# Optimization experiments

Hardware: AMD Instinct MI355X
Metric: run time of the kernel (lower is better)

Reference implementation:

```python
import jax, jax.numpy as jnp
import numpy as np

HID = (128, 256, 128)  # nmp_qc NNet hidden layer sizes
D_IN = 256
TARGET = 256


def _mlp_params(key, n_in, n_out, prefix):
    sizes = (n_in,) + HID + (n_out,)
    params = {}
    for i in range(len(sizes) - 1):
        key, k1, k2 = jax.random.split(key, 3)
        fan_in = sizes[i]
        bound = 1.0 / np.sqrt(fan_in)
        params[f"{prefix}_W{i}"] = jax.random.uniform(k1, (sizes[i], sizes[i + 1]), jnp.float32, -bound, bound)
        params[f"{prefix}_b{i}"] = jax.random.uniform(k2, (sizes[i + 1],), jnp.float32, -bound, bound)
    return params, key


def _mlp(x, Ws, bs):
    # ReLU on all layers except the last (linear output), matching NNet
    for i in range(len(Ws) - 1):
        x = jax.nn.relu(x @ Ws[i] + bs[i])
    return x @ Ws[-1] + bs[-1]


def setup_inputs() -> dict:
    key = jax.random.key(0)
    k0, k1, key = jax.random.split(key, 3)
    B, N = 512, 256
    inp = {
        "h0": jax.random.normal(k0, (B, N, D_IN), jnp.float32),
        "hT": jax.random.normal(k1, (B, N, D_IN), jnp.float32),
    }
    gp, key = _mlp_params(key, 2 * D_IN, TARGET, "g")  # gate MLP: concat(h0,hT) -> target
    op, key = _mlp_params(key, D_IN, TARGET, "o")      # value MLP: hT -> target
    inp.update(gp)
    inp.update(op)
    return inp


def reference(h0, hT,
              g_W0, g_b0, g_W1, g_b1, g_W2, g_b2, g_W3, g_b3,
              o_W0, o_b0, o_W1, o_b1, o_W2, o_b2, o_W3, o_b3):
    gWs = (g_W0, g_W1, g_W2, g_W3)
    gbs = (g_b0, g_b1, g_b2, g_b3)
    oWs = (o_W0, o_W1, o_W2, o_W3)
    obs = (o_b0, o_b1, o_b2, o_b3)
    # gate: sigmoid(MLP1([h0; hT])) ; value: MLP2(hT)  -- all [B, N, target]
    gate = jax.nn.sigmoid(_mlp(jnp.concatenate([h0, hT], axis=-1), gWs, gbs))
    val = _mlp(hT, oWs, obs)
    # node validity mask: sum of initial features > 0, matching r_mpnn
    mask = (jnp.sum(h0, axis=-1, keepdims=True) > 0).astype(h0.dtype)  # [B, N, 1]
    return jnp.sum(mask * gate * val, axis=1)  # [B, target]
```

## Files before the change

### kernel.cpp

```cpp
#include <hip/hip_runtime.h>
#include <hip/hip_bf16.h>
#include <stdint.h>


typedef __attribute__((ext_vector_type(8))) short short8_t;
typedef __attribute__((ext_vector_type(4))) float f32x4;

#define ROWS      48
#define TOTROWS   131072
#define NWG       2731

#define OFF_R     0
#define P_ELEMS   (48*136)
#define OFF_A     26112
#define OFF_B1    39168
#define OFF_MASK  63744
#define LDS_TOTAL 63936

__device__ __forceinline__ short f2bf(float f) {
  union { float f; uint32_t u; } v; v.f = f;
  uint32_t r = (v.u + 0x7FFFu + ((v.u >> 16) & 1u)) >> 16;
  return (short)r;
}
__device__ __forceinline__ float bf2f(short b) {
  union { uint32_t u; float f; } v; v.u = ((uint32_t)(uint16_t)b) << 16;
  return v.f;
}

template <int KTOT, int KSTEPS, int CT>
__device__ __forceinline__ void gemm_block(const short* __restrict__ actin, int Sin,
                                           const short* __restrict__ wsB, int kbaseB,
                                           f32x4 (&acc)[3][CT], int wv, int m, int q) {
#pragma unroll
  for (int ks = 0; ks < KSTEPS; ++ks) {
    const int kl = ks * 32 + q * 8;
    short8_t b[CT];
#pragma unroll
    for (int ct = 0; ct < CT; ++ct) {
      const int n = wv * (CT * 16) + ct * 16 + m;
      b[ct] = *(const short8_t*)(wsB + n * KTOT + kbaseB + kl);
    }
    short8_t a[3];
#pragma unroll
    for (int rt = 0; rt < 3; ++rt)
      a[rt] = *(const short8_t*)(actin + (rt * 16 + m) * Sin + kl);
#pragma unroll
    for (int ct = 0; ct < CT; ++ct)
#pragma unroll
      for (int rt = 0; rt < 3; ++rt)
        acc[rt][ct] = __builtin_amdgcn_mfma_f32_16x16x32_bf16(a[rt], b[ct], acc[rt][ct], 0, 0, 0);
  }
}

template <int N, int ACTF>
__device__ __forceinline__ void epilogue(f32x4 (&acc)[3][N / 64], short* actout, int Sout,
                                         const float* __restrict__ bias, int wv, int m, int q) {
  constexpr int CT = N / 64;
#pragma unroll
  for (int ct = 0; ct < CT; ++ct) {
    const int c = wv * (CT * 16) + ct * 16 + m;
    const float bv = bias[c];
#pragma unroll
    for (int rt = 0; rt < 3; ++rt)
#pragma unroll
      for (int i = 0; i < 4; ++i) {
        float v = acc[rt][ct][i] + bv;
        if (ACTF == 1) v = fmaxf(v, 0.f);
        if (ACTF == 2) v = 1.f / (1.f + __expf(-v));
        actout[(rt * 16 + q * 4 + i) * Sout + c] = f2bf(v);
      }
  }
}

template <int K, int N, int ACTF>
__device__ __forceinline__ void layer(const short* actin, int Sin, short* actout, int Sout,
                                      const short* __restrict__ wsB, const float* __restrict__ bias,
                                      int wv, int m, int q) {
  constexpr int CT = N / 64;
  f32x4 acc[3][CT];
#pragma unroll
  for (int rt = 0; rt < 3; ++rt)
#pragma unroll
    for (int ct = 0; ct < CT; ++ct) acc[rt][ct] = (f32x4)(0.f);
  gemm_block<K, K / 32, CT>(actin, Sin, wsB, 0, acc, wv, m, q);
  epilogue<N, ACTF>(acc, actout, Sout, bias, wv, m, q);
}

__device__ __forceinline__ void stage_load(const float* __restrict__ src, int row0, int colbase,
                                           int tid, float4 (&v)[6]) {
  const int c4 = tid & 31, rb = tid >> 5;
#pragma unroll
  for (int it = 0; it < 6; ++it) {
    int gr = row0 + rb + it * 8;
    if (gr >= TOTROWS) gr = TOTROWS - 1;
    v[it] = *(const float4*)(src + (size_t)gr * 256 + colbase + c4 * 4);
  }
}

__device__ __forceinline__ void stage_store(short* Pb, int tid, const float4 (&v)[6],
                                            float* maskacc, int mmode) {
  const int c4 = tid & 31, rb = tid >> 5;
#pragma unroll
  for (int it = 0; it < 6; ++it) {
    const int r = rb + it * 8;
    short4 pk; pk.x = f2bf(v[it].x); pk.y = f2bf(v[it].y); pk.z = f2bf(v[it].z); pk.w = f2bf(v[it].w);
    *(short4*)(Pb + r * 136 + c4 * 4) = pk;
    if (mmode) {
      float s = v[it].x + v[it].y + v[it].z + v[it].w;
      s += __shfl_down(s, 16, 32);
      s += __shfl_down(s, 8, 32);
      s += __shfl_down(s, 4, 32);
      s += __shfl_down(s, 2, 32);
      s += __shfl_down(s, 1, 32);
      if (c4 == 0) {
        if (mmode == 1) maskacc[r] = s; else maskacc[r] += s;
      }
    }
  }
}

template <int NCH, bool MASKA>
__device__ __forceinline__ void stream_layer(const float* __restrict__ src0,
                                             const float* __restrict__ src1, int splitc,
                                             const short* __restrict__ wsB,
                                             const float* __restrict__ bias,
                                             short* P, short* Aout, float* maskacc,
                                             int row0, int tid, int wv, int m, int q) {
  constexpr int KTOT = NCH * 128;
  f32x4 acc[3][2];
#pragma unroll
  for (int rt = 0; rt < 3; ++rt)
#pragma unroll
    for (int ct = 0; ct < 2; ++ct) acc[rt][ct] = (f32x4)(0.f);

  float4 v[6];
  stage_load(src0, row0, 0, tid, v);
  stage_store(P, tid, v, maskacc, MASKA ? 1 : 0);
  __syncthreads();
#pragma unroll
  for (int kc = 0; kc < NCH; ++kc) {
    const bool more = (kc + 1 < NCH);
    if (more) {
      const bool lo = (kc + 1 < splitc);
      stage_load(lo ? src0 : src1, row0, (lo ? (kc + 1) : (kc + 1 - splitc)) * 128, tid, v);
    }
    gemm_block<KTOT, 4, 2>(P + (kc & 1) * P_ELEMS, 136, wsB, kc * 128, acc, wv, m, q);
    if (more) {
      const int mm = (MASKA && (kc + 1 < splitc)) ? 2 : 0;
      stage_store(P + ((kc + 1) & 1) * P_ELEMS, tid, v, maskacc, mm);
    }
    __syncthreads();
  }
  epilogue<128, 1>(acc, Aout, 136, bias, wv, m, q);
}

__device__ __forceinline__ void final_layer(const short* actin, const short* __restrict__ wsB,
                                            const float* __restrict__ bias,
                                            const short* gateB, const float* maskacc,
                                            float* __restrict__ out, int row0,
                                            int wv, int m, int q) {
  f32x4 acc[3][4];
#pragma unroll
  for (int rt = 0; rt < 3; ++rt)
#pragma unroll
    for (int ct = 0; ct < 4; ++ct) acc[rt][ct] = (f32x4)(0.f);
  gemm_block<128, 4, 4>(actin, 136, wsB, 0, acc, wv, m, q);

  const int b0 = row0 >> 8;
  const int b1 = (row0 + ROWS - 1) >> 8;
#pragma unroll
  for (int ct = 0; ct < 4; ++ct) {
    const int c = wv * 64 + ct * 16 + m;
    const float bv = bias[c];
    float p0 = 0.f, p1 = 0.f;
#pragma unroll
    for (int rt = 0; rt < 3; ++rt)
#pragma unroll
      for (int i = 0; i < 4; ++i) {
        const int r = rt * 16 + q * 4 + i;
        const int gr = row0 + r;
        const float vv = acc[rt][ct][i] + bv;
        const float g = bf2f(gateB[r * 256 + c]);
        float contrib = (gr < TOTROWS && maskacc[r] > 0.f) ? g * vv : 0.f;
        if ((gr >> 8) == b0) p0 += contrib; else p1 += contrib;
      }
    p0 += __shfl_down(p0, 32); p0 += __shfl_down(p0, 16);
    p1 += __shfl_down(p1, 32); p1 += __shfl_down(p1, 16);
    if (q == 0) {
      atomicAdd(out + b0 * 256 + c, p0);
      if (b1 != b0 && b1 < 512) atomicAdd(out + b1 * 256 + c, p1);
    }
  }
}

__global__ __launch_bounds__(256, 2)
void readout_main(const float* __restrict__ h0, const float* __restrict__ hT,
                  const short* __restrict__ ws,
                  const float* __restrict__ gb0, const float* __restrict__ gb1,
                  const float* __restrict__ gb2, const float* __restrict__ gb3,
                  const float* __restrict__ ob0, const float* __restrict__ ob1,
                  const float* __restrict__ ob2, const float* __restrict__ ob3,
                  float* __restrict__ out) {
  __shared__ __align__(16) char smem[LDS_TOTAL];
  short* P  = (short*)(smem + OFF_R);
  short* B2 = (short*)(smem + OFF_R);
  short* A  = (short*)(smem + OFF_A);
  short* B1 = (short*)(smem + OFF_B1);
  float* maskacc = (float*)(smem + OFF_MASK);

  const int tid = threadIdx.x;
  const int wv = tid >> 6, lane = tid & 63;
  const int m = lane & 15, q = lane >> 4;
  const int row0 = blockIdx.x * ROWS;

  stream_layer<4, true>(h0, hT, 2, ws + 0, gb0, P, A, maskacc, row0, tid, wv, m, q);
  __syncthreads();
  layer<128, 256, 1>(A, 136, B2, 264, ws + 65536, gb1, wv, m, q);
  __syncthreads();
  layer<256, 128, 1>(B2, 264, A, 136, ws + 98304, gb2, wv, m, q);
  __syncthreads();
  layer<128, 256, 2>(A, 136, B1, 256, ws + 131072, gb3, wv, m, q);
  __syncthreads();
  stream_layer<2, false>(hT, hT, 2, ws + 163840, ob0, P, A, maskacc, row0, tid, wv, m, q);
  __syncthreads();
  layer<128, 256, 1>(A, 136, B2, 264, ws + 196608, ob1, wv, m, q);
  __syncthreads();
  layer<256, 128, 1>(B2, 264, A, 136, ws + 229376, ob2, wv, m, q);
  __syncthreads();
  final_layer(A, ws + 262144, ob3, B1, maskacc, out, row0, wv, m, q);
}

__global__ void prep(const float* __restrict__ W0, const float* __restrict__ W1,
                     const float* __restrict__ W2, const float* __restrict__ W3,
                     const float* __restrict__ W4, const float* __restrict__ W5,
                     const float* __restrict__ W6, const float* __restrict__ W7,
                     short* __restrict__ ws, float* __restrict__ out) {
  const int l = blockIdx.y;
  const int le = blockIdx.x * 256 + threadIdx.x;
  if (l == 1) { out[le] = 0.f; out[le + 65536] = 0.f; }
  int K, N, off; const float* W;
  switch (l) {
    case 0:  K = 512; N = 128; off = 0;      W = W0; break;
    case 1:  K = 128; N = 256; off = 65536;  W = W1; break;
    case 2:  K = 256; N = 128; off = 98304;  W = W2; break;
    case 3:  K = 128; N = 256; off = 131072; W = W3; break;
    case 4:  K = 256; N = 128; off = 163840; W = W4; break;
    case 5:  K = 128; N = 256; off = 196608; W = W5; break;
    case 6:  K = 256; N = 128; off = 229376; W = W6; break;
    default: K = 128; N = 256; off = 262144; W = W7; break;
  }
  if (le >= K * N) return;
  const int k = le / N, n = le % N;
  ws[off + n * K + k] = f2bf(W[le]);
}

extern "C" void kernel_launch(void* const* d_in, const int* in_sizes, int n_in,
                              void* d_out, int out_size, void* d_ws, size_t ws_size,
                              hipStream_t stream) {
  const float* h0  = (const float*)d_in[0];
  const float* hT  = (const float*)d_in[1];
  const float* gW0 = (const float*)d_in[2];  const float* gb0 = (const float*)d_in[3];
  const float* gW1 = (const float*)d_in[4];  const float* gb1 = (const float*)d_in[5];
  const float* gW2 = (const float*)d_in[6];  const float* gb2 = (const float*)d_in[7];
  const float* gW3 = (const float*)d_in[8];  const float* gb3 = (const float*)d_in[9];
  const float* oW0 = (const float*)d_in[10]; const float* ob0 = (const float*)d_in[11];
  const float* oW1 = (const float*)d_in[12]; const float* ob1 = (const float*)d_in[13];
  const float* oW2 = (const float*)d_in[14]; const float* ob2 = (const float*)d_in[15];
  const float* oW3 = (const float*)d_in[16]; const float* ob3 = (const float*)d_in[17];
  float* out = (float*)d_out;
  short* ws  = (short*)d_ws;

  prep<<<dim3(256, 8), 256, 0, stream>>>(gW0, gW1, gW2, gW3, oW0, oW1, oW2, oW3, ws, out);
  readout_main<<<NWG, 256, 0, stream>>>(h0, hT, ws,
                                        gb0, gb1, gb2, gb3,
                                        ob0, ob1, ob2, ob3, out);
}
```

Baseline: 520.8 us.

## Switch to 32x32 MFMA tiles, 64-row blocks, and keep gate output in registers

Result: faster. 483.3 us (-7.2%).

```diff
diff --git a/kernel.cpp b/kernel.cpp
--- a/kernel.cpp
+++ b/kernel.cpp
@@ -4,18 +4,16 @@
 
 
 typedef __attribute__((ext_vector_type(8))) short short8_t;
-typedef __attribute__((ext_vector_type(4))) float f32x4;
-
-#define ROWS      48
-#define TOTROWS   131072
-#define NWG       2731
-
-#define OFF_R     0
-#define P_ELEMS   (48*136)
-#define OFF_A     26112
-#define OFF_B1    39168
-#define OFF_MASK  63744
-#define LDS_TOTAL 63936
+typedef __attribute__((ext_vector_type(16))) float f32x16;
+
+#define ROWS 64
+#define NWG  2048
+
+#define PE        (64 * 136)
+#define OFF_P     0
+#define OFF_A     34816
+#define OFF_MASK  52224
+#define LDS_TOTAL 52480
 
 __device__ __forceinline__ short f2bf(float f) {
   union { float f; uint32_t u; } v; v.f = f;
@@ -28,80 +26,76 @@
 }
 
 template <int KTOT, int KSTEPS, int CT>
-__device__ __forceinline__ void gemm_block(const short* __restrict__ actin, int Sin,
-                                           const short* __restrict__ wsB, int kbaseB,
-                                           f32x4 (&acc)[3][CT], int wv, int m, int q) {
+__device__ __forceinline__ void gemm32(const short* actin, int Sin,
+                                       const short* __restrict__ wsB, int kw0, int c0,
+                                       f32x16 (&acc)[2][CT], int n32, int q32) {
 #pragma unroll
   for (int ks = 0; ks < KSTEPS; ++ks) {
-    const int kl = ks * 32 + q * 8;
+    const int kl = ks * 16 + q32 * 8;
     short8_t b[CT];
 #pragma unroll
-    for (int ct = 0; ct < CT; ++ct) {
-      const int n = wv * (CT * 16) + ct * 16 + m;
-      b[ct] = *(const short8_t*)(wsB + n * KTOT + kbaseB + kl);
-    }
-    short8_t a[3];
-#pragma unroll
-    for (int rt = 0; rt < 3; ++rt)
-      a[rt] = *(const short8_t*)(actin + (rt * 16 + m) * Sin + kl);
-#pragma unroll
     for (int ct = 0; ct < CT; ++ct)
-#pragma unroll
-      for (int rt = 0; rt < 3; ++rt)
-        acc[rt][ct] = __builtin_amdgcn_mfma_f32_16x16x32_bf16(a[rt], b[ct], acc[rt][ct], 0, 0, 0);
-  }
-}
-
-template <int N, int ACTF>
-__device__ __forceinline__ void epilogue(f32x4 (&acc)[3][N / 64], short* actout, int Sout,
-                                         const float* __restrict__ bias, int wv, int m, int q) {
-  constexpr int CT = N / 64;
+      b[ct] = *(const short8_t*)(wsB + (size_t)(c0 + ct * 32 + n32) * KTOT + kw0 + kl);
+    short8_t a[2];
+#pragma unroll
+    for (int rt = 0; rt < 2; ++rt)
+      a[rt] = *(const short8_t*)(actin + (rt * 32 + n32) * Sin + kl);
+#pragma unroll
+    for (int ct = 0; ct < CT; ++ct)
+#pragma unroll
+      for (int rt = 0; rt < 2; ++rt)
+        acc[rt][ct] = __builtin_amdgcn_mfma_f32_32x32x16_bf16(a[rt], b[ct], acc[rt][ct], 0, 0, 0);
+  }
+}
+
+template <int CT, int ACTF>
+__device__ __forceinline__ void epi32(f32x16 (&acc)[2][CT], short* actout, int Sout,
+                                      const float* __restrict__ bias, int c0, int n32, int q32) {
 #pragma unroll
   for (int ct = 0; ct < CT; ++ct) {
-    const int c = wv * (CT * 16) + ct * 16 + m;
+    const int c = c0 + ct * 32 + n32;
     const float bv = bias[c];
 #pragma unroll
-    for (int rt = 0; rt < 3; ++rt)
-#pragma unroll
-      for (int i = 0; i < 4; ++i) {
-        float v = acc[rt][ct][i] + bv;
+    for (int rt = 0; rt < 2; ++rt)
+#pragma unroll
+      for (int reg = 0; reg < 16; ++reg) {
+        const int r = rt * 32 + (reg & 3) + 8 * (reg >> 2) + 4 * q32;
+        float v = acc[rt][ct][reg] + bv;
         if (ACTF == 1) v = fmaxf(v, 0.f);
-        if (ACTF == 2) v = 1.f / (1.f + __expf(-v));
-        actout[(rt * 16 + q * 4 + i) * Sout + c] = f2bf(v);
+        actout[r * Sout + c] = f2bf(v);
       }
   }
 }
 
 template <int K, int N, int ACTF>
-__device__ __forceinline__ void layer(const short* actin, int Sin, short* actout, int Sout,
-                                      const short* __restrict__ wsB, const float* __restrict__ bias,
-                                      int wv, int m, int q) {
-  constexpr int CT = N / 64;
-  f32x4 acc[3][CT];
-#pragma unroll
-  for (int rt = 0; rt < 3; ++rt)
-#pragma unroll
-    for (int ct = 0; ct < CT; ++ct) acc[rt][ct] = (f32x4)(0.f);
-  gemm_block<K, K / 32, CT>(actin, Sin, wsB, 0, acc, wv, m, q);
-  epilogue<N, ACTF>(acc, actout, Sout, bias, wv, m, q);
+__device__ __forceinline__ void layer32(const short* actin, int Sin, short* actout, int Sout,
+                                        const short* __restrict__ wsB,
+                                        const float* __restrict__ bias,
+                                        int wv, int n32, int q32) {
+  constexpr int CT = N / 128;
+  const int c0 = wv * (N / 4);
+  f32x16 acc[2][CT];
+#pragma unroll
+  for (int rt = 0; rt < 2; ++rt)
+#pragma unroll
+    for (int ct = 0; ct < CT; ++ct) acc[rt][ct] = (f32x16)(0.f);
+  gemm32<K, K / 16, CT>(actin, Sin, wsB, 0, c0, acc, n32, q32);
+  epi32<CT, ACTF>(acc, actout, Sout, bias, c0, n32, q32);
 }
 
 __device__ __forceinline__ void stage_load(const float* __restrict__ src, int row0, int colbase,
-                                           int tid, float4 (&v)[6]) {
+                                           int tid, float4 (&v)[8]) {
   const int c4 = tid & 31, rb = tid >> 5;
 #pragma unroll
-  for (int it = 0; it < 6; ++it) {
-    int gr = row0 + rb + it * 8;
-    if (gr >= TOTROWS) gr = TOTROWS - 1;
-    v[it] = *(const float4*)(src + (size_t)gr * 256 + colbase + c4 * 4);
-  }
-}
-
-__device__ __forceinline__ void stage_store(short* Pb, int tid, const float4 (&v)[6],
+  for (int it = 0; it < 8; ++it)
+    v[it] = *(const float4*)(src + (size_t)(row0 + rb + it * 8) * 256 + colbase + c4 * 4);
+}
+
+__device__ __forceinline__ void stage_store(short* Pb, int tid, const float4 (&v)[8],
                                             float* maskacc, int mmode) {
   const int c4 = tid & 31, rb = tid >> 5;
 #pragma unroll
-  for (int it = 0; it < 6; ++it) {
+  for (int it = 0; it < 8; ++it) {
     const int r = rb + it * 8;
     short4 pk; pk.x = f2bf(v[it].x); pk.y = f2bf(v[it].y); pk.z = f2bf(v[it].z); pk.w = f2bf(v[it].w);
     *(short4*)(Pb + r * 136 + c4 * 4) = pk;
@@ -120,80 +114,93 @@
 }
 
 template <int NCH, bool MASKA>
-__device__ __forceinline__ void stream_layer(const float* __restrict__ src0,
-                                             const float* __restrict__ src1, int splitc,
-                                             const short* __restrict__ wsB,
-                                             const float* __restrict__ bias,
-                                             short* P, short* Aout, float* maskacc,
-                                             int row0, int tid, int wv, int m, int q) {
+__device__ __forceinline__ void stream32(const float* __restrict__ src0,
+                                         const float* __restrict__ src1, int splitc,
+                                         const short* __restrict__ wsB,
+                                         const float* __restrict__ bias,
+                                         short* P, short* Aout, float* maskacc,
+                                         int row0, int tid, int wv, int n32, int q32) {
   constexpr int KTOT = NCH * 128;
-  f32x4 acc[3][2];
-#pragma unroll
-  for (int rt = 0; rt < 3; ++rt)
-#pragma unroll
-    for (int ct = 0; ct < 2; ++ct) acc[rt][ct] = (f32x4)(0.f);
-
-  float4 v[6];
+  f32x16 acc[2][1];
+  acc[0][0] = (f32x16)(0.f); acc[1][0] = (f32x16)(0.f);
+  float4 v[8];
   stage_load(src0, row0, 0, tid, v);
   stage_store(P, tid, v, maskacc, MASKA ? 1 : 0);
   __syncthreads();
 #pragma unroll
   for (int kc = 0; kc < NCH; ++kc) {
-    const bool more = (kc + 1 < NCH);
-    if (more) {
+    if (kc + 1 < NCH) {
       const bool lo = (kc + 1 < splitc);
-      stage_load(lo ? src0 : src1, row0, (lo ? (kc + 1) : (kc + 1 - splitc)) * 128, tid, v);
+      stage_load(lo ? src0 : src1, row0, (lo ? kc + 1 : kc + 1 - splitc) * 128, tid, v);
     }
-    gemm_block<KTOT, 4, 2>(P + (kc & 1) * P_ELEMS, 136, wsB, kc * 128, acc, wv, m, q);
-    if (more) {
-      const int mm = (MASKA && (kc + 1 < splitc)) ? 2 : 0;
-      stage_store(P + ((kc + 1) & 1) * P_ELEMS, tid, v, maskacc, mm);
-    }
+    gemm32<KTOT, 8, 1>(P + (kc & 1) * PE, 136, wsB, kc * 128, wv * 32, acc, n32, q32);
+    if (kc + 1 < NCH)
+      stage_store(P + ((kc + 1) & 1) * PE, tid, v, maskacc, (MASKA && kc + 1 < splitc) ? 2 : 0);
     __syncthreads();
   }
-  epilogue<128, 1>(acc, Aout, 136, bias, wv, m, q);
-}
-
-__device__ __forceinline__ void final_layer(const short* actin, const short* __restrict__ wsB,
-                                            const float* __restrict__ bias,
-                                            const short* gateB, const float* maskacc,
-                                            float* __restrict__ out, int row0,
-                                            int wv, int m, int q) {
-  f32x4 acc[3][4];
-#pragma unroll
-  for (int rt = 0; rt < 3; ++rt)
-#pragma unroll
-    for (int ct = 0; ct < 4; ++ct) acc[rt][ct] = (f32x4)(0.f);
-  gemm_block<128, 4, 4>(actin, 136, wsB, 0, acc, wv, m, q);
-
-  const int b0 = row0 >> 8;
-  const int b1 = (row0 + ROWS - 1) >> 8;
-#pragma unroll
-  for (int ct = 0; ct < 4; ++ct) {
-    const int c = wv * 64 + ct * 16 + m;
+  epi32<1, 1>(acc, Aout, 136, bias, wv * 32, n32, q32);
+}
+
+__device__ __forceinline__ void gate_layer(const short* actin, const short* __restrict__ wsB,
+                                           const float* __restrict__ bias,
+                                           uint32_t (&gate)[2][2][8],
+                                           int wv, int n32, int q32) {
+  f32x16 acc[2][2];
+#pragma unroll
+  for (int rt = 0; rt < 2; ++rt)
+#pragma unroll
+    for (int ct = 0; ct < 2; ++ct) acc[rt][ct] = (f32x16)(0.f);
+  gemm32<128, 8, 2>(actin, 136, wsB, 0, wv * 64, acc, n32, q32);
+#pragma unroll
+  for (int ct = 0; ct < 2; ++ct) {
+    const float bv = bias[wv * 64 + ct * 32 + n32];
+#pragma unroll
+    for (int rt = 0; rt < 2; ++rt)
+#pragma unroll
+      for (int p = 0; p < 8; ++p) {
+        const float g0 = 1.f / (1.f + __expf(-(acc[rt][ct][2 * p] + bv)));
+        const float g1 = 1.f / (1.f + __expf(-(acc[rt][ct][2 * p + 1] + bv)));
+        gate[rt][ct][p] = ((uint32_t)(uint16_t)f2bf(g1) << 16) | (uint32_t)(uint16_t)f2bf(g0);
+      }
+  }
+}
+
+__device__ __forceinline__ void final32(const short* actin, const short* __restrict__ wsB,
+                                        const float* __restrict__ bias,
+                                        const uint32_t (&gate)[2][2][8],
+                                        const float* maskacc, float* __restrict__ out,
+                                        int row0, int wv, int n32, int q32, int lane) {
+  f32x16 acc[2][2];
+#pragma unroll
+  for (int rt = 0; rt < 2; ++rt)
+#pragma unroll
+    for (int ct = 0; ct < 2; ++ct) acc[rt][ct] = (f32x16)(0.f);
+  gemm32<128, 8, 2>(actin, 136, wsB, 0, wv * 64, acc, n32, q32);
+
+  const int b = row0 >> 8;
+#pragma unroll
+  for (int ct = 0; ct < 2; ++ct) {
+    const int c = wv * 64 + ct * 32 + n32;
     const float bv = bias[c];
-    float p0 = 0.f, p1 = 0.f;
-#pragma unroll
-    for (int rt = 0; rt < 3; ++rt)
-#pragma unroll
-      for (int i = 0; i < 4; ++i) {
-        const int r = rt * 16 + q * 4 + i;
-        const int gr = row0 + r;
-        const float vv = acc[rt][ct][i] + bv;
-        const float g = bf2f(gateB[r * 256 + c]);
-        float contrib = (gr < TOTROWS && maskacc[r] > 0.f) ? g * vv : 0.f;
-        if ((gr >> 8) == b0) p0 += contrib; else p1 += contrib;
-      }
-    p0 += __shfl_down(p0, 32); p0 += __shfl_down(p0, 16);
-    p1 += __shfl_down(p1, 32); p1 += __shfl_down(p1, 16);
-    if (q == 0) {
-      atomicAdd(out + b0 * 256 + c, p0);
-      if (b1 != b0 && b1 < 512) atomicAdd(out + b1 * 256 + c, p1);
-    }
-  }
-}
-
-__global__ __launch_bounds__(256, 2)
+    float s = 0.f;
+#pragma unroll
+    for (int rt = 0; rt < 2; ++rt)
+#pragma unroll
+      for (int p = 0; p < 8; ++p) {
+        const int r0 = rt * 32 + ((2 * p) & 3) + 8 * (p >> 1) + 4 * q32;
+        const float g0 = bf2f((short)(gate[rt][ct][p] & 0xFFFF));
+        const float g1 = bf2f((short)(gate[rt][ct][p] >> 16));
+        const float v0 = acc[rt][ct][2 * p] + bv;
+        const float v1 = acc[rt][ct][2 * p + 1] + bv;
+        if (maskacc[r0] > 0.f)     s += g0 * v0;
+        if (maskacc[r0 + 1] > 0.f) s += g1 * v1;
+      }
+    s += __shfl_down(s, 32);
+    if (lane < 32) atomicAdd(out + b * 256 + c, s);
+  }
+}
+
+__global__ __launch_bounds__(256, 3)
 void readout_main(const float* __restrict__ h0, const float* __restrict__ hT,
                   const short* __restrict__ ws,
                   const float* __restrict__ gb0, const float* __restrict__ gb1,
@@ -202,32 +209,31 @@
                   const float* __restrict__ ob2, const float* __restrict__ ob3,
                   float* __restrict__ out) {
   __shared__ __align__(16) char smem[LDS_TOTAL];
-  short* P  = (short*)(smem + OFF_R);
-  short* B2 = (short*)(smem + OFF_R);
+  short* P  = (short*)(smem + OFF_P);
+  short* B2 = (short*)(smem + OFF_P);
   short* A  = (short*)(smem + OFF_A);
-  short* B1 = (short*)(smem + OFF_B1);
   float* maskacc = (float*)(smem + OFF_MASK);
 
-  const int tid = threadIdx.x;
-  const int wv = tid >> 6, lane = tid & 63;
-  const int m = lane & 15, q = lane >> 4;
+  const int tid = threadIdx.x, lane = tid & 63, wv = tid >> 6;
+  const int n32 = lane & 31, q32 = lane >> 5;
   const int row0 = blockIdx.x * ROWS;
-
-  stream_layer<4, true>(h0, hT, 2, ws + 0, gb0, P, A, maskacc, row0, tid, wv, m, q);
-  __syncthreads();
-  layer<128, 256, 1>(A, 136, B2, 264, ws + 65536, gb1, wv, m, q);
-  __syncthreads();
-  layer<256, 128, 1>(B2, 264, A, 136, ws + 98304, gb2, wv, m, q);
-  __syncthreads();
-  layer<128, 256, 2>(A, 136, B1, 256, ws + 131072, gb3, wv, m, q);
-  __syncthreads();
-  stream_layer<2, false>(hT, hT, 2, ws + 163840, ob0, P, A, maskacc, row0, tid, wv, m, q);
-  __syncthreads();
-  layer<128, 256, 1>(A, 136, B2, 264, ws + 196608, ob1, wv, m, q);
-  __syncthreads();
-  layer<256, 128, 1>(B2, 264, A, 136, ws + 229376, ob2, wv, m, q);
-  __syncthreads();
-  final_layer(A, ws + 262144, ob3, B1, maskacc, out, row0, wv, m, q);
+  uint32_t gate[2][2][8];
+
+  stream32<4, true>(h0, hT, 2, ws + 0, gb0, P, A, maskacc, row0, tid, wv, n32, q32);
+  __syncthreads();
+  layer32<128, 256, 1>(A, 136, B2, 264, ws + 65536, gb1, wv, n32, q32);
+  __syncthreads();
+  layer32<256, 128, 1>(B2, 264, A, 136, ws + 98304, gb2, wv, n32, q32);
+  __syncthreads();
+  gate_layer(A, ws + 131072, gb3, gate, wv, n32, q32);
+  __syncthreads();
+  stream32<2, false>(hT, hT, 2, ws + 163840, ob0, P, A, maskacc, row0, tid, wv, n32, q32);
+  __syncthreads();
+  layer32<128, 256, 1>(A, 136, B2, 264, ws + 196608, ob1, wv, n32, q32);
+  __syncthreads();
+  layer32<256, 128, 1>(B2, 264, A, 136, ws + 229376, ob2, wv, n32, q32);
+  __syncthreads();
+  final32(A, ws + 262144, ob3, gate, maskacc, out, row0, wv, n32, q32, lane);
 }
 
 __global__ void prep(const float* __restrict__ W0, const float* __restrict__ W1,
```
